# Kernel optimization log

Measured on AMD Instinct MI355X. Metric: run time of the kernel, lower is better.

The kernel has to match this reference:

```python
import jax, jax.numpy as jnp
import numpy as np

B, T, D = 4096, 200, 64
H1, H2 = 64, 32


def _prelu(x, a):
    # PReLU with a single learnable slope (torch default num_parameters=1)
    return jnp.where(x >= 0, x, a * x)


def setup_inputs() -> dict:
    key = jax.random.key(0)
    ks = jax.random.split(key, 10)
    behavior = jax.random.normal(ks[0], (B, T, D), dtype=jnp.float32)
    candidate = jax.random.normal(ks[1], (B, D), dtype=jnp.float32)
    mask = jax.random.randint(ks[2], (B, T), 0, 2) > 0
    in_dim = 4 * D
    W1 = jax.random.normal(ks[3], (in_dim, H1), dtype=jnp.float32) / np.sqrt(in_dim)
    b1 = jnp.zeros((H1,), dtype=jnp.float32)
    a1 = jnp.full((1,), 0.25, dtype=jnp.float32)  # torch PReLU default init
    W2 = jax.random.normal(ks[4], (H1, H2), dtype=jnp.float32) / np.sqrt(H1)
    b2 = jnp.zeros((H2,), dtype=jnp.float32)
    a2 = jnp.full((1,), 0.25, dtype=jnp.float32)
    W3 = jax.random.normal(ks[5], (H2, 1), dtype=jnp.float32) / np.sqrt(H2)
    b3 = jnp.zeros((1,), dtype=jnp.float32)
    return {"behavior": behavior, "candidate": candidate, "mask": mask,
            "W1": W1, "b1": b1, "a1": a1,
            "W2": W2, "b2": b2, "a2": a2,
            "W3": W3, "b3": b3}


def reference(behavior, candidate, mask, W1, b1, a1, W2, b2, a2, W3, b3):
    # behavior: [B,T,D], candidate: [B,D], mask: [B,T] bool
    cand = candidate[:, None, :]                       # [B,1,D]
    cand_exp = jnp.broadcast_to(cand, behavior.shape)  # [B,T,D]
    diff = behavior - cand_exp
    prod = behavior * cand_exp
    att_input = jnp.concatenate([behavior, cand_exp, diff, prod], axis=-1)  # [B,T,4D]
    h = _prelu(att_input @ W1 + b1, a1)
    h = _prelu(h @ W2 + b2, a2)
    logits = (h @ W3 + b3)[..., 0]                     # [B,T]
    logits = jnp.where(mask, logits, -jnp.inf)
    w = jax.nn.softmax(logits, axis=-1)                # [B,T]
    user_interest = jnp.einsum('bt,btd->bd', w, behavior)  # [B,D]
    return user_interest
```

## Files before the change

kernel.cpp:

```cpp
#include <hip/hip_runtime.h>
#include <hip/hip_bf16.h>

#define T_LEN   200
#define NTILES  13
#define H0      7

typedef __bf16 bf16x8 __attribute__((ext_vector_type(8)));
typedef __bf16 bf16x4 __attribute__((ext_vector_type(4)));
typedef float  f32x4  __attribute__((ext_vector_type(4)));

#if __has_builtin(__builtin_amdgcn_mfma_f32_16x16x16_bf16)
#define MFMA16(a, b, c) __builtin_amdgcn_mfma_f32_16x16x16_bf16((a), (b), (c), 0, 0, 0)
#elif __has_builtin(__builtin_amdgcn_mfma_f32_16x16x16bf16_1k)
#define MFMA16(a, b, c) __builtin_amdgcn_mfma_f32_16x16x16bf16_1k((a), (b), (c), 0, 0, 0)
#else
static __device__ __forceinline__ f32x4 mfma16_asm(bf16x4 a, bf16x4 b, f32x4 c) {
  asm("v_mfma_f32_16x16x16_bf16 %0, %1, %2, %0" : "+v"(c) : "v"(a), "v"(b));
  return c;
}
#define MFMA16(a, b, c) mfma16_asm((a), (b), (c))
#endif

#define MFMA32(a, b, c) __builtin_amdgcn_mfma_f32_16x16x32_bf16((a), (b), (c), 0, 0, 0)

struct __align__(16) Smem {
  unsigned char w1ac[64 * 144];
  unsigned char w1d [64 * 144];
  float biasL[2][64];
  float mO[2][2][64];
  float mM[2][2];
  float mS[2][2];
};

__device__ __forceinline__ void loadA(const float* __restrict__ behB, int t, int kb,
                                      f32x4 (&x)[4]) {
  if (t < T_LEN) {
    const float* p = behB + (size_t)t * 64 + kb;
    x[0] = *(const f32x4*)p;
    x[1] = *(const f32x4*)(p + 4);
    x[2] = *(const f32x4*)(p + 32);
    x[3] = *(const f32x4*)(p + 36);
  } else {
    x[0] = f32x4{0.f, 0.f, 0.f, 0.f};
    x[1] = f32x4{0.f, 0.f, 0.f, 0.f};
    x[2] = f32x4{0.f, 0.f, 0.f, 0.f};
    x[3] = f32x4{0.f, 0.f, 0.f, 0.f};
  }
}

__global__ __launch_bounds__(256, 3) void lau_kernel(
    const float* __restrict__ behG, const float* __restrict__ candG,
    const int*  __restrict__ maskG,
    const float* __restrict__ W1g, const float* __restrict__ b1g, const float* __restrict__ a1g,
    const float* __restrict__ W2g, const float* __restrict__ b2g, const float* __restrict__ a2g,
    const float* __restrict__ W3g,
    float* __restrict__ outG)
{
  __shared__ Smem s;
  const int tid  = threadIdx.x;
  const int lane = tid & 63;
  const int wv   = tid >> 6;
  const int row  = wv >> 1;
  const int half = wv & 1;
  const int b    = blockIdx.x * 2 + row;
  const int r    = lane & 15;
  const int g    = lane >> 4;
  const int kb   = g * 8;

  for (int idx = tid; idx < 4096; idx += 256) {
    int j = idx & 63, d = idx >> 6;
    float ac = W1g[d * 64 + j] + W1g[(128 + d) * 64 + j];
    float dd = W1g[(192 + d) * 64 + j];
    *(__bf16*)(s.w1ac + j * 144 + d * 2) = (__bf16)ac;
    *(__bf16*)(s.w1d  + j * 144 + d * 2) = (__bf16)dd;
  }

  const float* candB = candG + (size_t)b * 64;

  if (half == 0) {
    float biasv = b1g[lane];
#pragma unroll 8
    for (int d = 0; d < 64; ++d) {
      float wd = W1g[(64 + d) * 64 + lane] - W1g[(128 + d) * 64 + lane];
      biasv += candB[d] * wd;
    }
    s.biasL[row][lane] = biasv;
  }
  __syncthreads();

  const bool boolmask = (__ballot(((const unsigned int*)maskG)[lane] > 1u) != 0ull);

  const f32x4 c0a = *(const f32x4*)(candB + kb);
  const f32x4 c0b = *(const f32x4*)(candB + kb + 4);
  const f32x4 c1a = *(const f32x4*)(candB + kb + 32);
  const f32x4 c1b = *(const f32x4*)(candB + kb + 36);

  bf16x8 A1[4][2];
#pragma unroll
  for (int f = 0; f < 8; ++f) {
    const int jt = f >> 1, kc = f & 1;
    const int rowoff = (jt * 16 + r) * 144 + kc * 64 + g * 16;
    bf16x8 ac = *(const bf16x8*)(s.w1ac + rowoff);
    bf16x8 dd = *(const bf16x8*)(s.w1d  + rowoff);
    f32x4 cA = kc ? c1a : c0a;
    f32x4 cB = kc ? c1b : c0b;
    bf16x8 o;
#pragma unroll
    for (int e = 0; e < 4; ++e) {
      o[e]     = (__bf16)((float)ac[e]     + cA[e] * (float)dd[e]);
      o[4 + e] = (__bf16)((float)ac[4 + e] + cB[e] * (float)dd[4 + e]);
    }
    A1[jt][kc] = o;
  }

  bf16x4 B2f[8];
#pragma unroll
  for (int f = 0; f < 8; ++f) {
    const int nt = f >> 2, c = f & 3;
#pragma unroll
    for (int i = 0; i < 4; ++i)
      B2f[f][i] = (__bf16)W2g[(c * 16 + g * 4 + i) * 32 + nt * 16 + r];
  }

  f32x4 bj4[4];
#pragma unroll
  for (int jt = 0; jt < 4; ++jt)
#pragma unroll
    for (int i = 0; i < 4; ++i)
      bj4[jt][i] = s.biasL[row][jt * 16 + g * 4 + i];

  const float al1 = a1g[0];
  const float al2 = a2g[0];
  const float b2v0 = b2g[r],  b2v1 = b2g[16 + r];
  const float w3v0 = W3g[r],  w3v1 = W3g[16 + r];
  const f32x4 cinit0 = {b2v0, b2v0, b2v0, b2v0};
  const f32x4 cinit1 = {b2v1, b2v1, b2v1, b2v1};

  const float* behB = behG + (size_t)b * T_LEN * 64;
  const unsigned char* maskB8 = (const unsigned char*)maskG + (size_t)b * T_LEN;
  const int* maskB32 = maskG + (size_t)b * T_LEN;

  const int mt0 = half ? H0 : 0;
  const int mtN = half ? (NTILES - H0) : H0;

  float mrun = -__builtin_inff();
  float srun = 0.f;
  f32x4 o0 = {0,0,0,0}, o1 = {0,0,0,0}, o2 = {0,0,0,0}, o3 = {0,0,0,0};

  f32x4 xc[4], xn[4];
  {
    int t0 = mt0 * 16 + r;
    loadA(behB, t0, kb, xc);
  }
  int mc = 0, mn = 0;
  {
    int t0 = mt0 * 16 + r;
    mc = (t0 < T_LEN) ? (boolmask ? (int)maskB8[t0] : maskB32[t0]) : 0;
  }

#pragma unroll 1
  for (int it = 0; it < mtN; ++it) {
    const int mt = mt0 + it;
    if (it + 1 < mtN) {
      int tn = (mt + 1) * 16 + r;
      loadA(behB, tn, kb, xn);
      mn = (tn < T_LEN) ? (boolmask ? (int)maskB8[tn] : maskB32[tn]) : 0;
    }

    bf16x8 ab0, ab1;
#pragma unroll
    for (int i = 0; i < 4; ++i) {
      ab0[i]     = (__bf16)xc[0][i];
      ab0[4 + i] = (__bf16)xc[1][i];
      ab1[i]     = (__bf16)xc[2][i];
      ab1[4 + i] = (__bf16)xc[3][i];
    }

    bf16x4 a2f[4];
#pragma unroll
    for (int jt = 0; jt < 4; ++jt) {
      f32x4 acc = MFMA32(A1[jt][0], ab0, bj4[jt]);
      acc = MFMA32(A1[jt][1], ab1, acc);
#pragma unroll
      for (int i = 0; i < 4; ++i) {
        float h = acc[i];
        h = (h >= 0.f) ? h : al1 * h;
        a2f[jt][i] = (__bf16)h;
      }
    }

    f32x4 acc20 = cinit0, acc21 = cinit1;
#pragma unroll
    for (int c = 0; c < 4; ++c) acc20 = MFMA16(a2f[c], B2f[c], acc20);
#pragma unroll
    for (int c = 0; c < 4; ++c) acc21 = MFMA16(a2f[c], B2f[4 + c], acc21);

    f32x4 q;
#pragma unroll
    for (int i = 0; i < 4; ++i) {
      float h0 = acc20[i]; h0 = (h0 >= 0.f) ? h0 : al2 * h0;
      float h1 = acc21[i]; h1 = (h1 >= 0.f) ? h1 : al2 * h1;
      q[i] = h0 * w3v0 + h1 * w3v1;
    }
#pragma unroll
    for (int off = 1; off < 16; off <<= 1)
#pragma unroll
      for (int i = 0; i < 4; ++i) q[i] += __shfl_xor(q[i], off);

    const int srcl = (r >> 2) << 4;
    float f0 = __shfl(q[0], srcl);
    float f1 = __shfl(q[1], srcl);
    float f2 = __shfl(q[2], srcl);
    float f3 = __shfl(q[3], srcl);
    float q01 = (r & 1) ? f1 : f0;
    float q23 = (r & 1) ? f3 : f2;
    float qt  = (r & 2) ? q23 : q01;

    const bool valid = ((mt * 16 + r) < T_LEN) && (mc != 0);
    float lvt = valid ? qt : -__builtin_inff();
    float tm = lvt;
#pragma unroll
    for (int off = 1; off < 16; off <<= 1) tm = fmaxf(tm, __shfl_xor(tm, off));

    if (tm > mrun + 8.f) {
      float fs = __expf(mrun - tm);
      srun *= fs;
#pragma unroll
      for (int i = 0; i < 4; ++i) { o0[i] *= fs; o1[i] *= fs; o2[i] *= fs; o3[i] *= fs; }
      mrun = tm;
    }
    float et = valid ? __expf(lvt - mrun) : 0.f;
    srun += et;
#pragma unroll
    for (int i = 0; i < 4; ++i) {
      o0[i] += et * xc[0][i];
      o1[i] += et * xc[1][i];
      o2[i] += et * xc[2][i];
      o3[i] += et * xc[3][i];
    }

#pragma unroll
    for (int i = 0; i < 4; ++i) xc[i] = xn[i];
    mc = mn;
  }

#pragma unroll
  for (int off = 1; off < 16; off <<= 1) {
#pragma unroll
    for (int i = 0; i < 4; ++i) {
      o0[i] += __shfl_xor(o0[i], off);
      o1[i] += __shfl_xor(o1[i], off);
      o2[i] += __shfl_xor(o2[i], off);
      o3[i] += __shfl_xor(o3[i], off);
    }
    srun += __shfl_xor(srun, off);
  }
  if (r == 0) {
    *(f32x4*)&s.mO[row][half][kb]      = o0;
    *(f32x4*)&s.mO[row][half][kb + 4]  = o1;
    *(f32x4*)&s.mO[row][half][kb + 32] = o2;
    *(f32x4*)&s.mO[row][half][kb + 36] = o3;
  }
  if (lane == 0) { s.mM[row][half] = mrun; s.mS[row][half] = srun; }
  __syncthreads();

  if (wv < 2) {
    const int rw = wv;
    const int bb = blockIdx.x * 2 + rw;
    float m0 = s.mM[rw][0], m1 = s.mM[rw][1];
    float M  = fmaxf(m0, m1);
    float e0 = __expf(m0 - M), e1 = __expf(m1 - M);
    float denom = s.mS[rw][0] * e0 + s.mS[rw][1] * e1;
    float inv = 1.f / denom;
    float val = (s.mO[rw][0][lane] * e0 + s.mO[rw][1][lane] * e1) * inv;
    outG[(size_t)bb * 64 + lane] = val;
  }
}

extern "C" void kernel_launch(void* const* d_in, const int* in_sizes, int n_in,
                              void* d_out, int out_size, void* d_ws, size_t ws_size,
                              hipStream_t stream) {
  (void)n_in; (void)d_ws; (void)ws_size; (void)out_size;
  const float* beh  = (const float*)d_in[0];
  const float* cand = (const float*)d_in[1];
  const int*   mask = (const int*)d_in[2];
  const float* W1   = (const float*)d_in[3];
  const float* b1   = (const float*)d_in[4];
  const float* a1   = (const float*)d_in[5];
  const float* W2   = (const float*)d_in[6];
  const float* b2   = (const float*)d_in[7];
  const float* a2   = (const float*)d_in[8];
  const float* W3   = (const float*)d_in[9];

  int B = in_sizes[1] / 64;
  int grid = B / 2;
  lau_kernel<<<grid, 256, 0, stream>>>(beh, cand, mask, W1, b1, a1, W2, b2, a2, W3,
                                       (float*)d_out);
}
```

Before: 60.64 us.

## Assign one batch row per wave and keep per-lane softmax state

Each wave now processes a full batch row over all 13 time tiles, so a block handles 4 rows instead of splitting one row across two waves. That removes the shared-memory merge and the second block barrier. The second MFMA is transposed (W2 as the A operand) so each lane receives logits for its own timestep, which replaces the long shuffle-and-select reduction with two xor shuffles. Online softmax state is tracked per lane and merged once at the end. The prefetch is restructured to reuse the bf16-converted values in the weighted sum, which lowers register use but uses bf16-rounded behavior values in the output accumulation and adds precision risk.

```diff
diff --git a/kernel.cpp b/kernel.cpp
--- a/kernel.cpp
+++ b/kernel.cpp
@@ -3,7 +3,6 @@
 
 #define T_LEN   200
 #define NTILES  13
-#define H0      7
 
 typedef __bf16 bf16x8 __attribute__((ext_vector_type(8)));
 typedef __bf16 bf16x4 __attribute__((ext_vector_type(4)));
@@ -26,10 +25,7 @@
 struct __align__(16) Smem {
   unsigned char w1ac[64 * 144];
   unsigned char w1d [64 * 144];
-  float biasL[2][64];
-  float mO[2][2][64];
-  float mM[2][2];
-  float mS[2][2];
+  float biasL[4][64];
 };
 
 __device__ __forceinline__ void loadA(const float* __restrict__ behB, int t, int kb,
@@ -60,12 +56,12 @@
   const int tid  = threadIdx.x;
   const int lane = tid & 63;
   const int wv   = tid >> 6;
-  const int row  = wv >> 1;
-  const int half = wv & 1;
-  const int b    = blockIdx.x * 2 + row;
+  const int b    = blockIdx.x * 4 + wv;
   const int r    = lane & 15;
   const int g    = lane >> 4;
   const int kb   = g * 8;
+
+  const float* candB = candG + (size_t)b * 64;
 
   for (int idx = tid; idx < 4096; idx += 256) {
     int j = idx & 63, d = idx >> 6;
@@ -74,17 +70,14 @@
     *(__bf16*)(s.w1ac + j * 144 + d * 2) = (__bf16)ac;
     *(__bf16*)(s.w1d  + j * 144 + d * 2) = (__bf16)dd;
   }
-
-  const float* candB = candG + (size_t)b * 64;
-
-  if (half == 0) {
+  {
     float biasv = b1g[lane];
 #pragma unroll 8
     for (int d = 0; d < 64; ++d) {
       float wd = W1g[(64 + d) * 64 + lane] - W1g[(128 + d) * 64 + lane];
       biasv += candB[d] * wd;
     }
-    s.biasL[row][lane] = biasv;
+    s.biasL[wv][lane] = biasv;
   }
   __syncthreads();
 
@@ -113,13 +106,13 @@
     A1[jt][kc] = o;
   }
 
-  bf16x4 B2f[8];
+  bf16x4 W2f[8];
 #pragma unroll
   for (int f = 0; f < 8; ++f) {
     const int nt = f >> 2, c = f & 3;
 #pragma unroll
     for (int i = 0; i < 4; ++i)
-      B2f[f][i] = (__bf16)W2g[(c * 16 + g * 4 + i) * 32 + nt * 16 + r];
+      W2f[f][i] = (__bf16)W2g[(c * 16 + g * 4 + i) * 32 + nt * 16 + r];
   }
 
   f32x4 bj4[4];
@@ -127,46 +120,29 @@
   for (int jt = 0; jt < 4; ++jt)
 #pragma unroll
     for (int i = 0; i < 4; ++i)
-      bj4[jt][i] = s.biasL[row][jt * 16 + g * 4 + i];
+      bj4[jt][i] = s.biasL[wv][jt * 16 + g * 4 + i];
 
   const float al1 = a1g[0];
   const float al2 = a2g[0];
-  const float b2v0 = b2g[r],  b2v1 = b2g[16 + r];
-  const float w3v0 = W3g[r],  w3v1 = W3g[16 + r];
-  const f32x4 cinit0 = {b2v0, b2v0, b2v0, b2v0};
-  const f32x4 cinit1 = {b2v1, b2v1, b2v1, b2v1};
+  const f32x4 cinit0 = *(const f32x4*)(b2g + g * 4);
+  const f32x4 cinit1 = *(const f32x4*)(b2g + 16 + g * 4);
+  const f32x4 w3f0   = *(const f32x4*)(W3g + g * 4);
+  const f32x4 w3f1   = *(const f32x4*)(W3g + 16 + g * 4);
 
   const float* behB = behG + (size_t)b * T_LEN * 64;
   const unsigned char* maskB8 = (const unsigned char*)maskG + (size_t)b * T_LEN;
   const int* maskB32 = maskG + (size_t)b * T_LEN;
 
-  const int mt0 = half ? H0 : 0;
-  const int mtN = half ? (NTILES - H0) : H0;
-
   float mrun = -__builtin_inff();
   float srun = 0.f;
   f32x4 o0 = {0,0,0,0}, o1 = {0,0,0,0}, o2 = {0,0,0,0}, o3 = {0,0,0,0};
 
-  f32x4 xc[4], xn[4];
-  {
-    int t0 = mt0 * 16 + r;
-    loadA(behB, t0, kb, xc);
-  }
-  int mc = 0, mn = 0;
-  {
-    int t0 = mt0 * 16 + r;
-    mc = (t0 < T_LEN) ? (boolmask ? (int)maskB8[t0] : maskB32[t0]) : 0;
-  }
+  f32x4 xc[4];
+  loadA(behB, r, kb, xc);
+  int mc = boolmask ? (int)maskB8[r] : maskB32[r];
 
 #pragma unroll 1
-  for (int it = 0; it < mtN; ++it) {
-    const int mt = mt0 + it;
-    if (it + 1 < mtN) {
-      int tn = (mt + 1) * 16 + r;
-      loadA(behB, tn, kb, xn);
-      mn = (tn < T_LEN) ? (boolmask ? (int)maskB8[tn] : maskB32[tn]) : 0;
-    }
-
+  for (int mt = 0; mt < NTILES; ++mt) {
     bf16x8 ab0, ab1;
 #pragma unroll
     for (int i = 0; i < 4; ++i) {
@@ -174,6 +150,12 @@
       ab0[4 + i] = (__bf16)xc[1][i];
       ab1[i]     = (__bf16)xc[2][i];
       ab1[4 + i] = (__bf16)xc[3][i];
+    }
+    const int mcur = mc;
+    if (mt + 1 < NTILES) {
+      int tn = (mt + 1) * 16 + r;
+      loadA(behB, tn, kb, xc);
+      mc = (tn < T_LEN) ? (boolmask ? (int)maskB8[tn] : maskB32[tn]) : 0;
     }
 
     bf16x4 a2f[4];
@@ -191,59 +173,49 @@
 
     f32x4 acc20 = cinit0, acc21 = cinit1;
 #pragma unroll
-    for (int c = 0; c < 4; ++c) acc20 = MFMA16(a2f[c], B2f[c], acc20);
-#pragma unroll
-    for (int c = 0; c < 4; ++c) acc21 = MFMA16(a2f[c], B2f[4 + c], acc21);
-
-    f32x4 q;
+    for (int c = 0; c < 4; ++c) acc20 = MFMA16(W2f[c],     a2f[c], acc20);
+#pragma unroll
+    for (int c = 0; c < 4; ++c) acc21 = MFMA16(W2f[4 + c], a2f[c], acc21);
+
+    float partial = 0.f;
 #pragma unroll
     for (int i = 0; i < 4; ++i) {
       float h0 = acc20[i]; h0 = (h0 >= 0.f) ? h0 : al2 * h0;
       float h1 = acc21[i]; h1 = (h1 >= 0.f) ? h1 : al2 * h1;
-      q[i] = h0 * w3v0 + h1 * w3v1;
-    }
-#pragma unroll
-    for (int off = 1; off < 16; off <<= 1)
-#pragma unroll
-      for (int i = 0; i < 4; ++i) q[i] += __shfl_xor(q[i], off);
-
-    const int srcl = (r >> 2) << 4;
-    float f0 = __shfl(q[0], srcl);
-    float f1 = __shfl(q[1], srcl);
-    float f2 = __shfl(q[2], srcl);
-    float f3 = __shfl(q[3], srcl);
-    float q01 = (r & 1) ? f1 : f0;
-    float q23 = (r & 1) ? f3 : f2;
-    float qt  = (r & 2) ? q23 : q01;
-
-    const bool valid = ((mt * 16 + r) < T_LEN) && (mc != 0);
-    float lvt = valid ? qt : -__builtin_inff();
-    float tm = lvt;
-#pragma unroll
-    for (int off = 1; off < 16; off <<= 1) tm = fmaxf(tm, __shfl_xor(tm, off));
-
-    if (tm > mrun + 8.f) {
-      float fs = __expf(mrun - tm);
+      partial += h0 * w3f0[i] + h1 * w3f1[i];
+    }
+    partial += __shfl_xor(partial, 16);
+    partial += __shfl_xor(partial, 32);
+
+    const bool valid = ((mt * 16 + r) < T_LEN) && (mcur != 0);
+    float lvt = valid ? partial : -__builtin_inff();
+    if (lvt > mrun + 8.f) {
+      float fs = __expf(mrun - lvt);
       srun *= fs;
 #pragma unroll
       for (int i = 0; i < 4; ++i) { o0[i] *= fs; o1[i] *= fs; o2[i] *= fs; o3[i] *= fs; }
-      mrun = tm;
+      mrun = lvt;
     }
     float et = valid ? __expf(lvt - mrun) : 0.f;
     srun += et;
 #pragma unroll
     for (int i = 0; i < 4; ++i) {
-      o0[i] += et * xc[0][i];
-      o1[i] += et * xc[1][i];
-      o2[i] += et * xc[2][i];
-      o3[i] += et * xc[3][i];
-    }
-
-#pragma unroll
-    for (int i = 0; i < 4; ++i) xc[i] = xn[i];
-    mc = mn;
-  }
-
+      o0[i] += et * (float)ab0[i];
+      o1[i] += et * (float)ab0[4 + i];
+      o2[i] += et * (float)ab1[i];
+      o3[i] += et * (float)ab1[4 + i];
+    }
+  }
+
+  float M = mrun;
+#pragma unroll
+  for (int off = 1; off < 16; off <<= 1) M = fmaxf(M, __shfl_xor(M, off));
+  {
+    float fac = __expf(mrun - M);
+    srun *= fac;
+#pragma unroll
+    for (int i = 0; i < 4; ++i) { o0[i] *= fac; o1[i] *= fac; o2[i] *= fac; o3[i] *= fac; }
+  }
 #pragma unroll
   for (int off = 1; off < 16; off <<= 1) {
 #pragma unroll
@@ -256,24 +228,16 @@
     srun += __shfl_xor(srun, off);
   }
   if (r == 0) {
-    *(f32x4*)&s.mO[row][half][kb]      = o0;
-    *(f32x4*)&s.mO[row][half][kb + 4]  = o1;
-    *(f32x4*)&s.mO[row][half][kb + 32] = o2;
-    *(f32x4*)&s.mO[row][half][kb + 36] = o3;
-  }
-  if (lane == 0) { s.mM[row][half] = mrun; s.mS[row][half] = srun; }
-  __syncthreads();
-
-  if (wv < 2) {
-    const int rw = wv;
-    const int bb = blockIdx.x * 2 + rw;
-    float m0 = s.mM[rw][0], m1 = s.mM[rw][1];
-    float M  = fmaxf(m0, m1);
-    float e0 = __expf(m0 - M), e1 = __expf(m1 - M);
-    float denom = s.mS[rw][0] * e0 + s.mS[rw][1] * e1;
-    float inv = 1.f / denom;
-    float val = (s.mO[rw][0][lane] * e0 + s.mO[rw][1][lane] * e1) * inv;
-    outG[(size_t)bb * 64 + lane] = val;
+    float inv = 1.f / srun;
+    float* po = outG + (size_t)b * 64 + kb;
+#pragma unroll
+    for (int i = 0; i < 4; ++i) {
+      o0[i] *= inv; o1[i] *= inv; o2[i] *= inv; o3[i] *= inv;
+    }
+    *(f32x4*)(po)      = o0;
+    *(f32x4*)(po + 4)  = o1;
+    *(f32x4*)(po + 32) = o2;
+    *(f32x4*)(po + 36) = o3;
   }
 }
 
@@ -293,7 +257,7 @@
   const float* W3   = (const float*)d_in[9];
 
   int B = in_sizes[1] / 64;
-  int grid = B / 2;
+  int grid = B / 4;
   lau_kernel<<<grid, 256, 0, stream>>>(beh, cand, mask, W1, b1, a1, W2, b2, a2, W3,
                                        (float*)d_out);
 }
```

New measurement: 58.61 us. -3.3%, faster.
